# Kernel optimization log

Measured on AMD Instinct MI355X. Metric: run time of the kernel, lower is better.

Reference implementation:

```python
import jax, jax.numpy as jnp
import numpy as np

B, T, DIN = 256, 2048, 3
H = 128
DOUT = 26


def _slstm_layer(x_seq, W, R, b):
    """sLSTM layer with exponential gating + log-domain stabilizer.
    x_seq: (B, T, Din); W: (4H, Din); R: (4H, H); b: (4H,). Returns (B, T, H)."""
    # input-driven gate preactivations for all timesteps at once
    gx = jnp.einsum('btd,gd->btg', x_seq, W) + b  # (B, T, 4H)
    gx = jnp.swapaxes(gx, 0, 1)                    # (T, B, 4H)
    Bsz = x_seq.shape[0]
    Hd = R.shape[1]
    z0 = jnp.zeros((Bsz, Hd), x_seq.dtype)

    def step(carry, gx_t):
        h, c, n, m = carry
        g = gx_t + h @ R.T                         # (B, 4H)
        it, ft, zt, ot = jnp.split(g, 4, axis=-1)
        m_new = jnp.maximum(ft + m, it)            # stabilizer state
        i = jnp.exp(it - m_new)                    # stabilized exp input gate
        f = jnp.exp(ft + m - m_new)                # stabilized exp forget gate
        z = jnp.tanh(zt)
        o = jax.nn.sigmoid(ot)
        c_new = f * c + i * z
        n_new = f * n + i                          # normalizer state
        h_new = o * (c_new / n_new)
        return (h_new, c_new, n_new, m_new), h_new

    (_, _, _, _), hs = jax.lax.scan(step, (z0, z0, z0, z0), gx)
    return jnp.swapaxes(hs, 0, 1)                  # (B, T, H)


def setup_inputs() -> dict:
    key = jax.random.key(0)
    ks = jax.random.split(key, 12)
    s = 0.1
    x = jax.random.normal(ks[0], (B, T, DIN), dtype=jnp.float32)
    W0 = jax.random.normal(ks[1], (4 * H, DIN), dtype=jnp.float32) * s
    R0 = jax.random.normal(ks[2], (4 * H, H), dtype=jnp.float32) * s
    b0 = jax.random.normal(ks[3], (4 * H,), dtype=jnp.float32) * s
    W1 = jax.random.normal(ks[4], (4 * H, H), dtype=jnp.float32) * s
    R1 = jax.random.normal(ks[5], (4 * H, H), dtype=jnp.float32) * s
    b1 = jax.random.normal(ks[6], (4 * H,), dtype=jnp.float32) * s
    Wmu = jax.random.normal(ks[7], (DOUT, H), dtype=jnp.float32) * s
    bmu = jax.random.normal(ks[8], (DOUT,), dtype=jnp.float32) * s
    Wsig = jax.random.normal(ks[9], (DOUT, H), dtype=jnp.float32) * s
    bsig = jax.random.normal(ks[10], (DOUT,), dtype=jnp.float32) * s
    return {"x": x, "W0": W0, "R0": R0, "b0": b0, "W1": W1, "R1": R1,
            "b1": b1, "Wmu": Wmu, "bmu": bmu, "Wsig": Wsig, "bsig": bsig}


def reference(x, W0, R0, b0, W1, R1, b1, Wmu, bmu, Wsig, bsig):
    h1 = _slstm_layer(x, W0, R0, b0)     # (B, T, H)
    h2 = _slstm_layer(h1, W1, R1, b1)    # (B, T, H)
    last = h2[:, -1, :]                  # (B, H); dropout is identity in eval
    mu = last @ Wmu.T + bmu
    sigma = jax.nn.softplus(last @ Wsig.T + bsig) + 1e-6
    return mu, sigma
```

## Files before the change

kernel.cpp:

```cpp
#include <hip/hip_runtime.h>
#include <cmath>

#define TT    2048
#define HH    128
#define NDIN  3
#define NDOUT 26
#define NTHR  512

typedef _Float16 f16x8 __attribute__((ext_vector_type(8)));
typedef float    f32x4 __attribute__((ext_vector_type(4)));

__device__ __forceinline__ float fast_rcp(float x){ return __builtin_amdgcn_rcpf(x); }

__device__ __forceinline__ f16x8 cvt8(const float* __restrict__ p){
    float4 a = *(const float4*)p;
    float4 b = *(const float4*)(p+4);
    f16x8 r;
    r[0]=(_Float16)a.x; r[1]=(_Float16)a.y; r[2]=(_Float16)a.z; r[3]=(_Float16)a.w;
    r[4]=(_Float16)b.x; r[5]=(_Float16)b.y; r[6]=(_Float16)b.z; r[7]=(_Float16)b.w;
    return r;
}

__global__
__attribute__((amdgpu_flat_work_group_size(NTHR, NTHR), amdgpu_waves_per_eu(2, 2)))
void slstm2_mfma(
    const float* __restrict__ x,
    const float* __restrict__ W0, const float* __restrict__ R0, const float* __restrict__ b0,
    const float* __restrict__ W1, const float* __restrict__ R1, const float* __restrict__ b1,
    const float* __restrict__ Wmu, const float* __restrict__ bmu,
    const float* __restrict__ Wsig, const float* __restrict__ bsig,
    float* __restrict__ out, int B)
{
    const int b    = blockIdx.x;
    const int tid  = threadIdx.x;
    const int wave = tid >> 6;
    const int lane = tid & 63;
    const int m    = lane & 15;
    const int g    = lane >> 4;

    __shared__ float xs[TT * NDIN];
    __shared__ __align__(16) _Float16 r1lds[32*64*8];
    __shared__ __align__(16) _Float16 hcat[2 * HH];
    __shared__ __align__(16) float g1q[HH * 4];
    __shared__ __align__(16) float g2q[HH * 4];
    __shared__ __align__(16) float w0g[4][HH * 4];
    __shared__ __align__(16) float b1qs[HH * 4];

    const float* xb = x + (size_t)b * (TT * NDIN);
    #pragma unroll
    for (int r = 0; r < (TT * NDIN) / NTHR; ++r)
        xs[r * NTHR + tid] = xb[r * NTHR + tid];

    if (tid < HH) {
        #pragma unroll
        for (int q = 0; q < 4; ++q) {
            w0g[q][tid*4+0] = W0[(q*HH + tid)*NDIN + 0];
            w0g[q][tid*4+1] = W0[(q*HH + tid)*NDIN + 1];
            w0g[q][tid*4+2] = W0[(q*HH + tid)*NDIN + 2];
            w0g[q][tid*4+3] = b0[q*HH + tid];
            b1qs[tid*4+q]   = b1[q*HH + tid];
        }
        hcat[tid] = (_Float16)0.f;
        hcat[HH + tid] = (_Float16)0.f;
    }

    #pragma unroll
    for (int it = 0; it < 4; ++it) {
        const int fid = tid + it * NTHR;
        const int l   = fid & 63;
        const int tau = fid >> 6;
        const int e   = tau*4 + ((l & 15) >> 2);
        const int q   = l & 3;
        const int gg  = l >> 4;
        *(f16x8*)(r1lds + (size_t)fid * 8) =
            cvt8(R1 + (size_t)(q*HH + e)*HH + 96 + gg*8);
    }

    f16x8 a1[4][4];
    f16x8 a2[4][7];
    #pragma unroll
    for (int tl = 0; tl < 4; ++tl) {
        const int e = (wave*4 + tl)*4 + (m >> 2);
        const int q = m & 3;
        const size_t row = (size_t)(q*HH + e);
        #pragma unroll
        for (int kt = 0; kt < 4; ++kt)
            a1[tl][kt] = cvt8(R0 + row*HH + kt*32 + g*8);
        #pragma unroll
        for (int kt = 0; kt < 4; ++kt)
            a2[tl][kt] = cvt8(W1 + row*HH + kt*32 + g*8);
        #pragma unroll
        for (int kt = 0; kt < 3; ++kt)
            a2[tl][4+kt] = cvt8(R1 + row*HH + kt*32 + g*8);
    }

    float c_s = 0.f, n_s = 0.f, m_s = 0.f;
    __syncthreads();

    for (int t = 0; t <= TT; ++t) {
        f16x8 bf[4];
        #pragma unroll
        for (int kt = 0; kt < 4; ++kt)
            bf[kt] = *(const f16x8*)(hcat + kt*32 + g*8);

        f32x4 cL[4];
        #pragma unroll
        for (int tl = 0; tl < 4; ++tl) cL[tl] = f32x4{0.f,0.f,0.f,0.f};
        #pragma unroll
        for (int kt = 0; kt < 4; ++kt) {
            #pragma unroll
            for (int tl = 0; tl < 4; ++tl)
                cL[tl] = __builtin_amdgcn_mfma_f32_16x16x32_f16(a1[tl][kt], bf[kt], cL[tl], 0, 0, 0);
        }
        if (m == 0) {
            #pragma unroll
            for (int tl = 0; tl < 4; ++tl)
                *(f32x4*)(g1q + ((wave*4 + tl)*4 + g)*4) = cL[tl];
        }

        #pragma unroll
        for (int tl = 0; tl < 4; ++tl) cL[tl] = f32x4{0.f,0.f,0.f,0.f};
        #pragma unroll
        for (int kt = 0; kt < 4; ++kt) {
            #pragma unroll
            for (int tl = 0; tl < 4; ++tl)
                cL[tl] = __builtin_amdgcn_mfma_f32_16x16x32_f16(a2[tl][kt], bf[kt], cL[tl], 0, 0, 0);
        }
        f16x8 bh[4];
        #pragma unroll
        for (int kt = 0; kt < 4; ++kt)
            bh[kt] = *(const f16x8*)(hcat + HH + kt*32 + g*8);
        f16x8 r1f[4];
        #pragma unroll
        for (int tl = 0; tl < 4; ++tl)
            r1f[tl] = *(const f16x8*)(r1lds + ((size_t)((wave*4 + tl)*64 + lane)) * 8);
        #pragma unroll
        for (int kt = 0; kt < 3; ++kt) {
            #pragma unroll
            for (int tl = 0; tl < 4; ++tl)
                cL[tl] = __builtin_amdgcn_mfma_f32_16x16x32_f16(a2[tl][4+kt], bh[kt], cL[tl], 0, 0, 0);
        }
        #pragma unroll
        for (int tl = 0; tl < 4; ++tl)
            cL[tl] = __builtin_amdgcn_mfma_f32_16x16x32_f16(r1f[tl], bh[3], cL[tl], 0, 0, 0);
        if (m == 0) {
            #pragma unroll
            for (int tl = 0; tl < 4; ++tl)
                *(f32x4*)(g2q + ((wave*4 + tl)*4 + g)*4) = cL[tl];
        }
        __syncthreads();

        if (t < TT && tid < HH) {
            f32x4 qd = *(const f32x4*)(g1q + tid*4);
            const float x0 = xs[t*3+0], x1 = xs[t*3+1], x2 = xs[t*3+2];
            f32x4 wi = *(const f32x4*)(&w0g[0][tid*4]);
            f32x4 wf = *(const f32x4*)(&w0g[1][tid*4]);
            f32x4 wz = *(const f32x4*)(&w0g[2][tid*4]);
            f32x4 wo = *(const f32x4*)(&w0g[3][tid*4]);
            const float it = qd[0] + wi[0]*x0 + wi[1]*x1 + wi[2]*x2 + wi[3];
            const float ft = qd[1] + wf[0]*x0 + wf[1]*x1 + wf[2]*x2 + wf[3];
            const float zt = qd[2] + wz[0]*x0 + wz[1]*x1 + wz[2]*x2 + wz[3];
            const float ot = qd[3] + wo[0]*x0 + wo[1]*x1 + wo[2]*x2 + wo[3];
            const float mn = fmaxf(ft + m_s, it);
            const float iv = __expf(it - mn);
            const float fv = __expf(ft + m_s - mn);
            const float tq = __expf(-2.f * fabsf(zt));
            float zv = (1.f - tq) * fast_rcp(1.f + tq);
            zv = (zt < 0.f) ? -zv : zv;
            const float ov = fast_rcp(1.f + __expf(-ot));
            c_s = fv * c_s + iv * zv;
            n_s = fv * n_s + iv;
            m_s = mn;
            hcat[tid] = (_Float16)(ov * (c_s * fast_rcp(n_s)));
        } else if (t > 0 && tid >= HH && tid < 2*HH) {
            const int e = tid - HH;
            f32x4 qd = *(const f32x4*)(g2q + e*4);
            f32x4 bb = *(const f32x4*)(b1qs + e*4);
            const float it = qd[0] + bb[0];
            const float ft = qd[1] + bb[1];
            const float zt = qd[2] + bb[2];
            const float ot = qd[3] + bb[3];
            const float mn = fmaxf(ft + m_s, it);
            const float iv = __expf(it - mn);
            const float fv = __expf(ft + m_s - mn);
            const float tq = __expf(-2.f * fabsf(zt));
            float zv = (1.f - tq) * fast_rcp(1.f + tq);
            zv = (zt < 0.f) ? -zv : zv;
            const float ov = fast_rcp(1.f + __expf(-ot));
            c_s = fv * c_s + iv * zv;
            n_s = fv * n_s + iv;
            m_s = mn;
            hcat[HH + e] = (_Float16)(ov * (c_s * fast_rcp(n_s)));
        }
        __syncthreads();
    }

    if (tid < 2 * NDOUT) {
        const int d = (tid < NDOUT) ? tid : (tid - NDOUT);
        const float* Wr = ((tid < NDOUT) ? Wmu : Wsig) + (size_t)d * HH;
        float acc = (tid < NDOUT) ? bmu[d] : bsig[d];
        #pragma unroll 8
        for (int k = 0; k < HH; ++k) acc += (float)hcat[HH + k] * Wr[k];
        if (tid < NDOUT) {
            out[(size_t)b * NDOUT + d] = acc;
        } else {
            const float sp = fmaxf(acc, 0.f) + log1pf(__expf(-fabsf(acc)));
            out[(size_t)B * NDOUT + (size_t)b * NDOUT + d] = sp + 1e-6f;
        }
    }
}

extern "C" void kernel_launch(void* const* d_in, const int* in_sizes, int n_in,
                              void* d_out, int out_size, void* d_ws, size_t ws_size,
                              hipStream_t stream) {
    const float* x    = (const float*)d_in[0];
    const float* W0   = (const float*)d_in[1];
    const float* R0   = (const float*)d_in[2];
    const float* b0   = (const float*)d_in[3];
    const float* W1   = (const float*)d_in[4];
    const float* R1   = (const float*)d_in[5];
    const float* b1   = (const float*)d_in[6];
    const float* Wmu  = (const float*)d_in[7];
    const float* bmu  = (const float*)d_in[8];
    const float* Wsig = (const float*)d_in[9];
    const float* bsig = (const float*)d_in[10];
    float* out = (float*)d_out;

    const int B = in_sizes[0] / (TT * NDIN);

    slstm2_mfma<<<B, NTHR, 0, stream>>>(x, W0, R0, b0, W1, R1, b1,
                                        Wmu, bmu, Wsig, bsig, out, B);
}
```

Baseline: 2.744 ms.

## Compute gate updates in MFMA lanes with double-buffered hidden state, one barrier

Each wave now applies the sLSTM gate nonlinearities straight from its MFMA accumulator lanes instead of staging gate pre-activations through LDS and handing them to 256 dedicated threads. The hidden state is double-buffered, so each timestep needs one barrier instead of two. The layer-0 input projection uses packed fp16 dot2 with weights held in registers, and the weight fragments are pinned to AGPRs with inline asm. This is meant to cut LDS round-trips and barrier latency on the serial critical path. In exchange, every lane redundantly evaluates the gate math, and the input projection loses some precision from running in fp16.

```diff
diff --git a/kernel.cpp b/kernel.cpp
--- a/kernel.cpp
+++ b/kernel.cpp
@@ -7,10 +7,14 @@
 #define NDOUT 26
 #define NTHR  512
 
+typedef _Float16 h2t  __attribute__((ext_vector_type(2)));
 typedef _Float16 f16x8 __attribute__((ext_vector_type(8)));
 typedef float    f32x4 __attribute__((ext_vector_type(4)));
 
 __device__ __forceinline__ float fast_rcp(float x){ return __builtin_amdgcn_rcpf(x); }
+__device__ __forceinline__ float fdot2(h2t a, h2t b, float c){
+    return __builtin_amdgcn_fdot2(a, b, c, false);
+}
 
 __device__ __forceinline__ f16x8 cvt8(const float* __restrict__ p){
     float4 a = *(const float4*)p;
@@ -19,6 +23,21 @@
     r[0]=(_Float16)a.x; r[1]=(_Float16)a.y; r[2]=(_Float16)a.z; r[3]=(_Float16)a.w;
     r[4]=(_Float16)b.x; r[5]=(_Float16)b.y; r[6]=(_Float16)b.z; r[7]=(_Float16)b.w;
     return r;
+}
+
+__device__ __forceinline__ float slstm_up(float it, float ft, float zt, float ot,
+                                          float& c_s, float& n_s, float& m_s){
+    const float mn = fmaxf(ft + m_s, it);
+    const float iv = __expf(it - mn);
+    const float fv = __expf(ft + m_s - mn);
+    const float tq = __expf(-2.f * fabsf(zt));
+    float zv = (1.f - tq) * fast_rcp(1.f + tq);
+    zv = (zt < 0.f) ? -zv : zv;
+    const float ov = fast_rcp(1.f + __expf(-ot));
+    c_s = fv * c_s + iv * zv;
+    n_s = fv * n_s + iv;
+    m_s = mn;
+    return ov * (c_s * fast_rcp(n_s));
 }
 
 __global__
@@ -37,32 +56,20 @@
     const int lane = tid & 63;
     const int m    = lane & 15;
     const int g    = lane >> 4;
+    const int tls  = lane & 3;
+    const int eu   = (wave*4 + tls)*4 + g;
+    const bool wr  = ((lane >> 2) & 3) == 0;
 
     __shared__ float xs[TT * NDIN];
     __shared__ __align__(16) _Float16 r1lds[32*64*8];
-    __shared__ __align__(16) _Float16 hcat[2 * HH];
-    __shared__ __align__(16) float g1q[HH * 4];
-    __shared__ __align__(16) float g2q[HH * 4];
-    __shared__ __align__(16) float w0g[4][HH * 4];
-    __shared__ __align__(16) float b1qs[HH * 4];
+    __shared__ __align__(16) _Float16 hbuf[2][2*HH];
 
     const float* xb = x + (size_t)b * (TT * NDIN);
     #pragma unroll
     for (int r = 0; r < (TT * NDIN) / NTHR; ++r)
         xs[r * NTHR + tid] = xb[r * NTHR + tid];
 
-    if (tid < HH) {
-        #pragma unroll
-        for (int q = 0; q < 4; ++q) {
-            w0g[q][tid*4+0] = W0[(q*HH + tid)*NDIN + 0];
-            w0g[q][tid*4+1] = W0[(q*HH + tid)*NDIN + 1];
-            w0g[q][tid*4+2] = W0[(q*HH + tid)*NDIN + 2];
-            w0g[q][tid*4+3] = b0[q*HH + tid];
-            b1qs[tid*4+q]   = b1[q*HH + tid];
-        }
-        hcat[tid] = (_Float16)0.f;
-        hcat[HH + tid] = (_Float16)0.f;
-    }
+    if (tid < 2*HH) { hbuf[0][tid] = (_Float16)0.f; hbuf[1][tid] = (_Float16)0.f; }
 
     #pragma unroll
     for (int it = 0; it < 4; ++it) {
@@ -76,6 +83,16 @@
             cvt8(R1 + (size_t)(q*HH + e)*HH + 96 + gg*8);
     }
 
+    h2t w0p[4], w0q[4];
+    float b1v[4];
+    #pragma unroll
+    for (int q = 0; q < 4; ++q) {
+        const float* wrow = W0 + (size_t)(q*HH + eu) * NDIN;
+        w0p[q] = h2t{(_Float16)wrow[0], (_Float16)wrow[1]};
+        w0q[q] = h2t{(_Float16)wrow[2], (_Float16)b0[q*HH + eu]};
+        b1v[q] = b1[q*HH + eu];
+    }
+
     f16x8 a1[4][4];
     f16x8 a2[4][7];
     #pragma unroll
@@ -84,123 +101,98 @@
         const int q = m & 3;
         const size_t row = (size_t)(q*HH + e);
         #pragma unroll
-        for (int kt = 0; kt < 4; ++kt)
+        for (int kt = 0; kt < 4; ++kt) {
             a1[tl][kt] = cvt8(R0 + row*HH + kt*32 + g*8);
-        #pragma unroll
-        for (int kt = 0; kt < 4; ++kt)
+            asm("" : "+a"(a1[tl][kt]));
+        }
+        #pragma unroll
+        for (int kt = 0; kt < 4; ++kt) {
             a2[tl][kt] = cvt8(W1 + row*HH + kt*32 + g*8);
-        #pragma unroll
-        for (int kt = 0; kt < 3; ++kt)
+            asm("" : "+a"(a2[tl][kt]));
+        }
+        #pragma unroll
+        for (int kt = 0; kt < 3; ++kt) {
             a2[tl][4+kt] = cvt8(R1 + row*HH + kt*32 + g*8);
-    }
-
-    float c_s = 0.f, n_s = 0.f, m_s = 0.f;
+            asm("" : "+a"(a2[tl][4+kt]));
+        }
+    }
+
+    float c1 = 0.f, n1 = 0.f, m1 = 0.f;
+    float c2 = 0.f, n2 = 0.f, m2 = 0.f;
     __syncthreads();
 
     for (int t = 0; t <= TT; ++t) {
-        f16x8 bf[4];
-        #pragma unroll
-        for (int kt = 0; kt < 4; ++kt)
-            bf[kt] = *(const f16x8*)(hcat + kt*32 + g*8);
+        const _Float16* hprev = hbuf[(t + 1) & 1];
+        _Float16*       hcur  = hbuf[t & 1];
 
         f32x4 cL[4];
         #pragma unroll
         for (int tl = 0; tl < 4; ++tl) cL[tl] = f32x4{0.f,0.f,0.f,0.f};
         #pragma unroll
         for (int kt = 0; kt < 4; ++kt) {
-            #pragma unroll
-            for (int tl = 0; tl < 4; ++tl)
-                cL[tl] = __builtin_amdgcn_mfma_f32_16x16x32_f16(a1[tl][kt], bf[kt], cL[tl], 0, 0, 0);
-        }
-        if (m == 0) {
-            #pragma unroll
-            for (int tl = 0; tl < 4; ++tl)
-                *(f32x4*)(g1q + ((wave*4 + tl)*4 + g)*4) = cL[tl];
-        }
-
-        #pragma unroll
-        for (int tl = 0; tl < 4; ++tl) cL[tl] = f32x4{0.f,0.f,0.f,0.f};
-        #pragma unroll
-        for (int kt = 0; kt < 4; ++kt) {
-            #pragma unroll
-            for (int tl = 0; tl < 4; ++tl)
-                cL[tl] = __builtin_amdgcn_mfma_f32_16x16x32_f16(a2[tl][kt], bf[kt], cL[tl], 0, 0, 0);
-        }
-        f16x8 bh[4];
-        #pragma unroll
-        for (int kt = 0; kt < 4; ++kt)
-            bh[kt] = *(const f16x8*)(hcat + HH + kt*32 + g*8);
-        f16x8 r1f[4];
-        #pragma unroll
-        for (int tl = 0; tl < 4; ++tl)
-            r1f[tl] = *(const f16x8*)(r1lds + ((size_t)((wave*4 + tl)*64 + lane)) * 8);
+            f16x8 bf = *(const f16x8*)(hprev + kt*32 + g*8);
+            #pragma unroll
+            for (int tl = 0; tl < 4; ++tl)
+                cL[tl] = __builtin_amdgcn_mfma_f32_16x16x32_f16(a1[tl][kt], bf, cL[tl], 0, 0, 0);
+        }
+        if (t < TT) {
+            f32x4 s01 = (lane & 1) ? cL[1] : cL[0];
+            f32x4 s23 = (lane & 1) ? cL[3] : cL[2];
+            f32x4 qd  = (lane & 2) ? s23 : s01;
+            const h2t xp = h2t{(_Float16)xs[t*3+0], (_Float16)xs[t*3+1]};
+            const h2t xq = h2t{(_Float16)xs[t*3+2], (_Float16)1.0f};
+            const float it = fdot2(w0p[0], xp, fdot2(w0q[0], xq, qd[0]));
+            const float ft = fdot2(w0p[1], xp, fdot2(w0q[1], xq, qd[1]));
+            const float zt = fdot2(w0p[2], xp, fdot2(w0q[2], xq, qd[2]));
+            const float ot = fdot2(w0p[3], xp, fdot2(w0q[3], xq, qd[3]));
+            const float hv = slstm_up(it, ft, zt, ot, c1, n1, m1);
+            if (wr) hcur[eu] = (_Float16)hv;
+        }
+
+        f32x4 cM[4];
+        #pragma unroll
+        for (int tl = 0; tl < 4; ++tl) cM[tl] = f32x4{0.f,0.f,0.f,0.f};
+        #pragma unroll
+        for (int kt = 0; kt < 4; ++kt) {
+            f16x8 bf = *(const f16x8*)(hprev + kt*32 + g*8);
+            #pragma unroll
+            for (int tl = 0; tl < 4; ++tl)
+                cM[tl] = __builtin_amdgcn_mfma_f32_16x16x32_f16(a2[tl][kt], bf, cM[tl], 0, 0, 0);
+        }
         #pragma unroll
         for (int kt = 0; kt < 3; ++kt) {
-            #pragma unroll
-            for (int tl = 0; tl < 4; ++tl)
-                cL[tl] = __builtin_amdgcn_mfma_f32_16x16x32_f16(a2[tl][4+kt], bh[kt], cL[tl], 0, 0, 0);
-        }
-        #pragma unroll
-        for (int tl = 0; tl < 4; ++tl)
-            cL[tl] = __builtin_amdgcn_mfma_f32_16x16x32_f16(r1f[tl], bh[3], cL[tl], 0, 0, 0);
-        if (m == 0) {
-            #pragma unroll
-            for (int tl = 0; tl < 4; ++tl)
-                *(f32x4*)(g2q + ((wave*4 + tl)*4 + g)*4) = cL[tl];
-        }
-        __syncthreads();
-
-        if (t < TT && tid < HH) {
-            f32x4 qd = *(const f32x4*)(g1q + tid*4);
-            const float x0 = xs[t*3+0], x1 = xs[t*3+1], x2 = xs[t*3+2];
-            f32x4 wi = *(const f32x4*)(&w0g[0][tid*4]);
-            f32x4 wf = *(const f32x4*)(&w0g[1][tid*4]);
-            f32x4 wz = *(const f32x4*)(&w0g[2][tid*4]);
-            f32x4 wo = *(const f32x4*)(&w0g[3][tid*4]);
-            const float it = qd[0] + wi[0]*x0 + wi[1]*x1 + wi[2]*x2 + wi[3];
-            const float ft = qd[1] + wf[0]*x0 + wf[1]*x1 + wf[2]*x2 + wf[3];
-            const float zt = qd[2] + wz[0]*x0 + wz[1]*x1 + wz[2]*x2 + wz[3];
-            const float ot = qd[3] + wo[0]*x0 + wo[1]*x1 + wo[2]*x2 + wo[3];
-            const float mn = fmaxf(ft + m_s, it);
-            const float iv = __expf(it - mn);
-            const float fv = __expf(ft + m_s - mn);
-            const float tq = __expf(-2.f * fabsf(zt));
-            float zv = (1.f - tq) * fast_rcp(1.f + tq);
-            zv = (zt < 0.f) ? -zv : zv;
-            const float ov = fast_rcp(1.f + __expf(-ot));
-            c_s = fv * c_s + iv * zv;
-            n_s = fv * n_s + iv;
-            m_s = mn;
-            hcat[tid] = (_Float16)(ov * (c_s * fast_rcp(n_s)));
-        } else if (t > 0 && tid >= HH && tid < 2*HH) {
-            const int e = tid - HH;
-            f32x4 qd = *(const f32x4*)(g2q + e*4);
-            f32x4 bb = *(const f32x4*)(b1qs + e*4);
-            const float it = qd[0] + bb[0];
-            const float ft = qd[1] + bb[1];
-            const float zt = qd[2] + bb[2];
-            const float ot = qd[3] + bb[3];
-            const float mn = fmaxf(ft + m_s, it);
-            const float iv = __expf(it - mn);
-            const float fv = __expf(ft + m_s - mn);
-            const float tq = __expf(-2.f * fabsf(zt));
-            float zv = (1.f - tq) * fast_rcp(1.f + tq);
-            zv = (zt < 0.f) ? -zv : zv;
-            const float ov = fast_rcp(1.f + __expf(-ot));
-            c_s = fv * c_s + iv * zv;
-            n_s = fv * n_s + iv;
-            m_s = mn;
-            hcat[HH + e] = (_Float16)(ov * (c_s * fast_rcp(n_s)));
+            f16x8 bh = *(const f16x8*)(hprev + HH + kt*32 + g*8);
+            #pragma unroll
+            for (int tl = 0; tl < 4; ++tl)
+                cM[tl] = __builtin_amdgcn_mfma_f32_16x16x32_f16(a2[tl][4+kt], bh, cM[tl], 0, 0, 0);
+        }
+        {
+            f16x8 bh3 = *(const f16x8*)(hprev + HH + 96 + g*8);
+            f16x8 r1f[4];
+            #pragma unroll
+            for (int tl = 0; tl < 4; ++tl)
+                r1f[tl] = *(const f16x8*)(r1lds + ((size_t)(wave*4 + tl)*64 + lane) * 8);
+            #pragma unroll
+            for (int tl = 0; tl < 4; ++tl)
+                cM[tl] = __builtin_amdgcn_mfma_f32_16x16x32_f16(r1f[tl], bh3, cM[tl], 0, 0, 0);
+        }
+        if (t > 0) {
+            f32x4 s01 = (lane & 1) ? cM[1] : cM[0];
+            f32x4 s23 = (lane & 1) ? cM[3] : cM[2];
+            f32x4 qd  = (lane & 2) ? s23 : s01;
+            const float hv = slstm_up(qd[0] + b1v[0], qd[1] + b1v[1],
+                                      qd[2] + b1v[2], qd[3] + b1v[3], c2, n2, m2);
+            if (wr) hcur[HH + eu] = (_Float16)hv;
         }
         __syncthreads();
     }
 
     if (tid < 2 * NDOUT) {
         const int d = (tid < NDOUT) ? tid : (tid - NDOUT);
-        const float* Wr = ((tid < NDOUT) ? Wmu : Wsig) + (size_t)d * HH;
+        const float* Wr2 = ((tid < NDOUT) ? Wmu : Wsig) + (size_t)d * HH;
         float acc = (tid < NDOUT) ? bmu[d] : bsig[d];
         #pragma unroll 8
-        for (int k = 0; k < HH; ++k) acc += (float)hcat[HH + k] * Wr[k];
+        for (int k = 0; k < HH; ++k) acc += (float)hbuf[0][HH + k] * Wr2[k];
         if (tid < NDOUT) {
             out[(size_t)b * NDOUT + d] = acc;
         } else {
```

After: 2.778 ms. Within noise of the previous version (+1.2%).
